# Kernel optimization log

Measured on AMD Instinct MI355X. Metric: run time of the kernel, lower is better.

## Reference

```python
import jax, jax.numpy as jnp
import numpy as np
import math

B, L, D, H = 4, 1024, 512, 8
TAU = 0.1
LN_EPS = 1e-5


def _attn(xq, xk, xv, wq, bq, wk, bk, wv, bv, wo, bo, energy=None, threshold=None):
    Bq, Lq, Dm = xq.shape
    Dh = Dm // H
    Q = (xq @ wq.T + bq).reshape(Bq, Lq, H, Dh)
    K = (xk @ wk.T + bk).reshape(Bq, -1, H, Dh)
    V = (xv @ wv.T + bv).reshape(Bq, -1, H, Dh)
    sc = jnp.einsum('bqhd,bkhd->bhqk', Q, K) / jnp.sqrt(jnp.float32(Dh))
    if energy is not None:
        # mask keys whose mean |energy| over channels is below threshold
        mask = jnp.abs(energy).mean(-1)[:, None, None, :] > threshold  # (B,1,1,Lk)
        sc = jnp.where(mask, sc, -jnp.inf)
    w = jnp.nan_to_num(jax.nn.softmax(sc, axis=-1))  # nan->0 for fully-masked rows
    o = jnp.einsum('bhqk,bkhd->bqhd', w, V).reshape(Bq, Lq, Dm)
    return o @ wo.T + bo


def _ln(x, w, b):
    m = x.mean(-1, keepdims=True)
    v = x.var(-1, keepdims=True)
    return (x - m) / jnp.sqrt(v + LN_EPS) * w + b


def _mlp(x, w1, b1, w2, b2):
    h = jax.nn.gelu(x @ w1.T + b1, approximate=False)  # torch nn.GELU default = exact
    return h @ w2.T + b2


def setup_inputs():
    key = jax.random.key(0)
    ks = list(jax.random.split(key, 64))

    def nxt():
        return ks.pop(0)

    def w(shape, scale=0.02):
        return jax.random.normal(nxt(), shape, dtype=jnp.float32) * scale

    inp = {
        'LL': jax.random.normal(nxt(), (B, D, L), dtype=jnp.float32),
        'LH': jax.random.normal(nxt(), (B, D, L), dtype=jnp.float32),
        'raw_tau': jnp.float32(math.log(TAU / (1.0 - TAU))),
    }
    for p in ('llA', 'lhA', 'crA'):
        for nm in ('q', 'k', 'v', 'o'):
            inp[f'{p}_w{nm}'] = w((D, D))
            inp[f'{p}_b{nm}'] = jnp.zeros((D,), jnp.float32)
    for p in ('mlp_ll', 'mlp_lh'):
        inp[f'{p}_w1'] = w((4 * D, D))
        inp[f'{p}_b1'] = jnp.zeros((4 * D,), jnp.float32)
        inp[f'{p}_w2'] = w((D, 4 * D))
        inp[f'{p}_b2'] = jnp.zeros((D,), jnp.float32)
    inp['n1_w'] = jnp.ones((D,), jnp.float32)
    inp['n1_b'] = jnp.zeros((D,), jnp.float32)
    inp['n2_w'] = jnp.ones((D,), jnp.float32)
    inp['n2_b'] = jnp.zeros((D,), jnp.float32)
    return inp


def reference(LL, LH, raw_tau,
              llA_wq, llA_bq, llA_wk, llA_bk, llA_wv, llA_bv, llA_wo, llA_bo,
              lhA_wq, lhA_bq, lhA_wk, lhA_bk, lhA_wv, lhA_bv, lhA_wo, lhA_bo,
              crA_wq, crA_bq, crA_wk, crA_bk, crA_wv, crA_bv, crA_wo, crA_bo,
              mlp_ll_w1, mlp_ll_b1, mlp_ll_w2, mlp_ll_b2,
              mlp_lh_w1, mlp_lh_b1, mlp_lh_w2, mlp_lh_b2,
              n1_w, n1_b, n2_w, n2_b):
    tau = jax.nn.sigmoid(raw_tau)
    ll_s = jnp.transpose(LL, (0, 2, 1))  # (B,L,D)
    lh_s = jnp.transpose(LH, (0, 2, 1))
    ll_o = _attn(ll_s, ll_s, ll_s, llA_wq, llA_bq, llA_wk, llA_bk, llA_wv, llA_bv, llA_wo, llA_bo)
    lh_o = _attn(lh_s, lh_s, lh_s, lhA_wq, lhA_bq, lhA_wk, lhA_bk, lhA_wv, lhA_bv, lhA_wo, lhA_bo,
                 energy=lh_s, threshold=tau)
    cr_o = _attn(ll_o, lh_o, lh_o, crA_wq, crA_bq, crA_wk, crA_bk, crA_wv, crA_bv, crA_wo, crA_bo)
    ll_f = _ln(ll_s + ll_o + cr_o, n1_w, n1_b)
    ll_f = _mlp(ll_f, mlp_ll_w1, mlp_ll_b1, mlp_ll_w2, mlp_ll_b2) + ll_f
    lh_f = _ln(lh_s + lh_o, n2_w, n2_b)
    lh_f = _mlp(lh_f, mlp_lh_w1, mlp_lh_b1, mlp_lh_w2, mlp_lh_b2) + lh_f
    return (jnp.transpose(ll_f, (0, 2, 1)), jnp.transpose(lh_f, (0, 2, 1)))
```

## Files before the change

### kernel.cpp

```cpp
#include <hip/hip_runtime.h>
#include <hip/hip_bf16.h>
#include <stdint.h>

typedef unsigned short u16;
typedef __bf16 bf16_t;
typedef bf16_t bf16x8 __attribute__((ext_vector_type(8)));
typedef float f32x4 __attribute__((ext_vector_type(4)));

#define DEV static __device__ __forceinline__

DEV u16 f2b(float f) {
    __hip_bfloat16 h = __float2bfloat16(f);
    return __builtin_bit_cast(u16, h);
}

DEV bf16x8 ld_frag(const u16* p) {
    uint4 u = *reinterpret_cast<const uint4*>(p);
    return __builtin_bit_cast(bf16x8, u);
}

DEV float gelu(float v) {
    float y = 0.79788456080286536f * (v + 0.044715f * v * v * v);
    float e = __expf(-2.f * fabsf(y));
    float th = (1.f - e) / (1.f + e);
    th = copysignf(th, y);
    return 0.5f * v * (1.f + th);
}

DEV void gl_lds16(const u16* g, u16* l) {
    __builtin_amdgcn_global_load_lds(
        (const __attribute__((address_space(1))) void*)(uintptr_t)g,
        (__attribute__((address_space(3))) void*)(unsigned int)(uintptr_t)l,
        16, 0, 0);
}

struct ConvEnt { const float* s; u16* d; int n; };
struct ConvArgs { ConvEnt e[16]; };

__global__ __launch_bounds__(256) void k_conv(ConvArgs a) {
    const ConvEnt en = a.e[blockIdx.y];
    for (int i = (blockIdx.x * 256 + threadIdx.x) * 4; i < en.n; i += 256 * 256 * 4) {
        const float4 f = *reinterpret_cast<const float4*>(en.s + i);
        unsigned r0 = (unsigned)f2b(f.x) | ((unsigned)f2b(f.y) << 16);
        unsigned r1 = (unsigned)f2b(f.z) | ((unsigned)f2b(f.w) << 16);
        uint2 rr; rr.x = r0; rr.y = r1;
        *reinterpret_cast<uint2*>(en.d + i) = rr;
    }
}

struct CpyEnt { const float* s; float* d; };
struct CpyArgs { CpyEnt e[8]; };

__global__ __launch_bounds__(256) void k_cpyf(CpyArgs a) {
    const CpyEnt en = a.e[blockIdx.y];
    int i = blockIdx.x * 256 + threadIdx.x;
    en.d[i] = en.s[i];
}

__global__ __launch_bounds__(256) void k_tin(const float* __restrict__ LL, const float* __restrict__ LH,
                                             float* __restrict__ llf, u16* __restrict__ llb,
                                             float* __restrict__ lhf, u16* __restrict__ lhb) {
    __shared__ float t[32][33];
    int z = blockIdx.z, b = z & 3;
    const float* in = (z < 4) ? LL : LH;
    float* of = (z < 4) ? llf : lhf;
    u16* ob = (z < 4) ? llb : lhb;
    int l0 = blockIdx.x * 32, d0 = blockIdx.y * 32;
    int tx = threadIdx.x, ty = threadIdx.y;
#pragma unroll
    for (int j = 0; j < 4; ++j) {
        int d = d0 + ty + j * 8;
        t[ty + j * 8][tx] = in[((size_t)b * 512 + d) * 1024 + l0 + tx];
    }
    __syncthreads();
#pragma unroll
    for (int j = 0; j < 4; ++j) {
        int l = l0 + ty + j * 8;
        float v = t[tx][ty + j * 8];
        size_t o = ((size_t)b * 1024 + l) * 512 + d0 + tx;
        of[o] = v;
        ob[o] = f2b(v);
    }
}

__global__ __launch_bounds__(256) void k_tout(const float* __restrict__ y0, const float* __restrict__ y1,
                                              float* __restrict__ out) {
    __shared__ float t[32][33];
    int z = blockIdx.z, b = z & 3;
    const float* in = (z < 4) ? y0 : y1;
    float* o = out + ((z < 4) ? 0 : (size_t)4096 * 512);
    int l0 = blockIdx.x * 32, d0 = blockIdx.y * 32;
    int tx = threadIdx.x, ty = threadIdx.y;
#pragma unroll
    for (int j = 0; j < 4; ++j) {
        int l = l0 + ty + j * 8;
        t[ty + j * 8][tx] = in[((size_t)b * 1024 + l) * 512 + d0 + tx];
    }
    __syncthreads();
#pragma unroll
    for (int j = 0; j < 4; ++j) {
        int d = d0 + ty + j * 8;
        o[((size_t)b * 512 + d) * 1024 + l0 + tx] = t[tx][ty + j * 8];
    }
}

__global__ __launch_bounds__(256) void k_mask(const float* __restrict__ lh_s,
                                              const float* __restrict__ raw_tau,
                                              float* __restrict__ kbias) {
    int row = blockIdx.x * 4 + (threadIdx.x >> 6);
    int lane = threadIdx.x & 63;
    const float* p = lh_s + (size_t)row * 512 + lane * 8;
    float s = 0.f;
#pragma unroll
    for (int j = 0; j < 8; ++j) s += fabsf(p[j]);
#pragma unroll
    for (int m = 32; m >= 1; m >>= 1) s += __shfl_xor(s, m, 64);
    float tau = 1.f / (1.f + expf(-raw_tau[0]));
    if (lane == 0) kbias[row] = (s * (1.f / 512.f) > tau) ? 0.f : -3.0e38f;
}

__global__ __launch_bounds__(256) void k_ln(const float* __restrict__ a, const float* __restrict__ b,
                                            const float* __restrict__ c, const float* __restrict__ w,
                                            const float* __restrict__ bi,
                                            float* __restrict__ of, u16* __restrict__ ob) {
    int row = blockIdx.x * 4 + (threadIdx.x >> 6);
    int lane = threadIdx.x & 63;
    size_t base = (size_t)row * 512 + lane * 8;
    float x[8];
#pragma unroll
    for (int j = 0; j < 8; ++j) {
        float v = a[base + j] + b[base + j];
        if (c) v += c[base + j];
        x[j] = v;
    }
    float s = 0.f, s2 = 0.f;
#pragma unroll
    for (int j = 0; j < 8; ++j) { s += x[j]; s2 += x[j] * x[j]; }
#pragma unroll
    for (int m = 32; m >= 1; m >>= 1) { s += __shfl_xor(s, m, 64); s2 += __shfl_xor(s2, m, 64); }
    float mean = s * (1.f / 512.f);
    float var = s2 * (1.f / 512.f) - mean * mean;
    float rs = rsqrtf(var + 1e-5f);
#pragma unroll
    for (int j = 0; j < 8; ++j) {
        float y = (x[j] - mean) * rs * w[lane * 8 + j] + bi[lane * 8 + j];
        of[base + j] = y;
        ob[base + j] = f2b(y);
    }
}

struct GP {
    const u16* A; const u16* W; const float* bias; const float* res;
    float* Cf; u16* Cb; u16* Qp; u16* Kp; u16* Vt;
    int N, K, kB, vB, nwg;
};

template <int BM, int BN, int GELU_ACT, int PACK>
__global__ __launch_bounds__(256) void k_gemm(GP p0, GP p1, int M) {
    constexpr int BK = 64;
    __shared__ alignas(16) u16 Al[2][BM * BK];
    __shared__ alignas(16) u16 Wl[2][BN * BK];
    GP g = (blockIdx.y == 0) ? p0 : p1;
    const int orig = blockIdx.x;
    if (orig >= g.nwg) return;
    int bid;
    {
        const int xcd = orig & 7, lin = orig >> 3;
        const int q = g.nwg >> 3, r = g.nwg & 7;
        bid = (xcd < r ? xcd * (q + 1) : r * (q + 1) + (xcd - r) * q) + lin;
    }
    const int K = g.K, N = g.N;
    const int nny = N / BN;
    const int m0 = (bid / nny) * BM, n0 = (bid % nny) * BN;

    const int t = threadIdx.x, w = t >> 6, l = t & 63;
    constexpr int FM = BM / 32, FN = BN / 32;
    const int wr = w >> 1, wc = w & 1;
    const int lq = l & 15, lg = l >> 4;
    f32x4 acc[FM][FN] = {};

    const int srow = l >> 3, schunk = l & 7;
    auto stage = [&](int kcol, int buf) {
#pragma unroll
        for (int i = 0; i < BM / 32; ++i) {
            const int row = i * 32 + w * 8 + srow;
            gl_lds16(g.A + (size_t)(m0 + row) * K + kcol + ((schunk ^ (row & 7)) * 8),
                     &Al[buf][(i * 32 + w * 8) * BK]);
        }
#pragma unroll
        for (int i = 0; i < BN / 32; ++i) {
            const int row = i * 32 + w * 8 + srow;
            gl_lds16(g.W + (size_t)(n0 + row) * K + kcol + ((schunk ^ (row & 7)) * 8),
                     &Wl[buf][(i * 32 + w * 8) * BK]);
        }
    };

    stage(0, 0);
    const int KT = K / BK;
    for (int kt = 0; kt < KT; ++kt) {
        const int cur = kt & 1;
        __syncthreads();
        if (kt + 1 < KT) stage((kt + 1) * BK, cur ^ 1);
#pragma unroll
        for (int s = 0; s < 2; ++s) {
            bf16x8 af[FM], bw[FN];
#pragma unroll
            for (int i = 0; i < FM; ++i) {
                const int row = wr * (BM / 2) + i * 16 + lq;
                af[i] = ld_frag(&Al[cur][row * BK + (((s * 4 + lg) ^ (row & 7)) * 8)]);
            }
#pragma unroll
            for (int j = 0; j < FN; ++j) {
                const int row = wc * (BN / 2) + j * 16 + lq;
                bw[j] = ld_frag(&Wl[cur][row * BK + (((s * 4 + lg) ^ (row & 7)) * 8)]);
            }
#pragma unroll
            for (int i = 0; i < FM; ++i)
#pragma unroll
                for (int j = 0; j < FN; ++j)
                    acc[i][j] = __builtin_amdgcn_mfma_f32_16x16x32_bf16(af[i], bw[j], acc[i][j], 0, 0, 0);
        }
    }

    if (PACK && n0 >= g.vB) {
        u16* T = (u16*)Al;
        constexpr int CH = BM / 8, CMASK = CH - 1, SH = (CH == 16) ? 4 : 3;
        __syncthreads();
#pragma unroll
        for (int i = 0; i < FM; ++i) {
#pragma unroll
            for (int j = 0; j < FN; ++j) {
                const int ni = wc * (BN / 2) + j * 16 + lq;
                const float bn = g.bias[n0 + ni];
#pragma unroll
                for (int r2 = 0; r2 < 4; ++r2) {
                    const int mi = wr * (BM / 2) + i * 16 + lg * 4 + r2;
                    T[ni * BM + (((mi >> 3) ^ (ni & CMASK)) * 8) + (mi & 7)] = f2b(acc[i][j][r2] + bn);
                }
            }
        }
        __syncthreads();
        const int bb = m0 >> 10, mloc = m0 & 1023;
        const int mc = t & CMASK, nib = t >> SH;
        constexpr int RPP = 256 / CH;
#pragma unroll
        for (int p2 = 0; p2 < BN / RPP; ++p2) {
            const int ni = nib + p2 * RPP;
            uint4 u = *reinterpret_cast<const uint4*>(&T[ni * BM + ((mc ^ (ni & CMASK)) * 8)]);
            const int d = n0 - g.vB + ni;
            *reinterpret_cast<uint4*>(
                &g.Vt[((size_t)(bb * 8 + (d >> 6)) * 64 + (d & 63)) * 1024 + mloc + mc * 8]) = u;
        }
        return;
    }

#pragma unroll
    for (int i = 0; i < FM; ++i) {
#pragma unroll
        for (int j = 0; j < FN; ++j) {
            const int n = n0 + wc * (BN / 2) + j * 16 + lq;
            const float bn = g.bias[n];
#pragma unroll
            for (int r2 = 0; r2 < 4; ++r2) {
                const int m = m0 + wr * (BM / 2) + i * 16 + lg * 4 + r2;
                float v = acc[i][j][r2] + bn;
                if (GELU_ACT) v = gelu(v);
                if (PACK) {
                    const int bb = m >> 10, ll_ = m & 1023;
                    if (n >= g.kB) {
                        const int d = n - g.kB;
                        g.Kp[((size_t)(bb * 8 + (d >> 6)) * 1024 + ll_) * 64 + (d & 63)] = f2b(v);
                    } else {
                        g.Qp[((size_t)(bb * 8 + (n >> 6)) * 1024 + ll_) * 64 + (n & 63)] = f2b(v * 0.125f);
                    }
                } else {
                    size_t o = (size_t)m * N + n;
                    if (g.res) v += g.res[o];
                    if (g.Cf) g.Cf[o] = v;
                    if (g.Cb) g.Cb[o] = f2b(v);
                }
            }
        }
    }
}

__global__ __launch_bounds__(256) void k_attn(const u16* __restrict__ Qp, const u16* __restrict__ Kp,
                                              const u16* __restrict__ Vtp, u16* __restrict__ O,
                                              const float* __restrict__ kbias, int nwg) {
    constexpr int L = 1024;
    __shared__ alignas(16) u16 Kl[2][64 * 64];
    __shared__ alignas(16) u16 Vl[2][64 * 64];
    __shared__ alignas(16) u16 Pl[128 * 64];
    const int t = threadIdx.x, w = t >> 6, l = t & 63;
    const int bid = ((int)blockIdx.x & 7) * (nwg >> 3) + ((int)blockIdx.x >> 3);
    const int bh = bid >> 3, q0 = (bid & 7) * 128;
    const int bz = bh >> 3, h = bh & 7;
    const int lq = l & 15, lg = l >> 4;
    const float* kb = (kbias != nullptr && bz >= 4) ? (kbias + (size_t)(bz - 4) * L) : nullptr;

    bf16x8 qa[2][2];
#pragma unroll
    for (int i = 0; i < 2; ++i) {
        const u16* qp = Qp + ((size_t)bh * L + q0 + w * 32 + i * 16 + lq) * 64 + lg * 8;
        qa[i][0] = ld_frag(qp);
        qa[i][1] = ld_frag(qp + 32);
    }

    const int r0 = w * 16 + (l >> 3), r1 = r0 + 8, c = l & 7;
    const u16* Ksrc0 = Kp + (size_t)bh * L * 64 + (size_t)r0 * 64 + ((c ^ (r0 & 7)) * 8);
    const u16* Ksrc1 = Kp + (size_t)bh * L * 64 + (size_t)r1 * 64 + ((c ^ (r1 & 7)) * 8);
    const u16* Vsrc0 = Vtp + (size_t)bh * 64 * L + (size_t)r0 * L + ((c ^ (r0 & 7)) * 8);
    const u16* Vsrc1 = Vtp + (size_t)bh * 64 * L + (size_t)r1 * L + ((c ^ (r1 & 7)) * 8);

    auto stage = [&](int k0, int buf) {
        gl_lds16(Ksrc0 + (size_t)k0 * 64, &Kl[buf][(w * 16) * 64]);
        gl_lds16(Ksrc1 + (size_t)k0 * 64, &Kl[buf][(w * 16 + 8) * 64]);
        gl_lds16(Vsrc0 + k0, &Vl[buf][(w * 16) * 64]);
        gl_lds16(Vsrc1 + k0, &Vl[buf][(w * 16 + 8) * 64]);
    };

    int addrA[4][2];
#pragma unroll
    for (int f = 0; f < 4; ++f) {
        int row = f * 16 + lq;
#pragma unroll
        for (int s = 0; s < 2; ++s) addrA[f][s] = row * 64 + (((s * 4 + lg) ^ (row & 7)) * 8);
    }
    int paddr[2][2], pwbase[2];
#pragma unroll
    for (int i = 0; i < 2; ++i) {
        const int prow = w * 32 + i * 16 + lq;
#pragma unroll
        for (int s = 0; s < 2; ++s) paddr[i][s] = prow * 64 + (((s * 4 + lg) ^ (prow & 7)) * 8);
        pwbase[i] = w * 32 + i * 16 + lg * 4;
    }

    f32x4 oacc[2][4] = {};
    float lrow[2][4] = {};

    stage(0, 0);
    for (int kt = 0; kt < 16; ++kt) {
        const int cur = kt & 1;
        __syncthreads();
        if (kt + 1 < 16) stage((kt + 1) * 64, cur ^ 1);

        f32x4 sc[2][4];
#pragma unroll
        for (int f = 0; f < 4; ++f) {
            bf16x8 k0 = ld_frag(&Kl[cur][addrA[f][0]]);
            bf16x8 k1 = ld_frag(&Kl[cur][addrA[f][1]]);
#pragma unroll
            for (int i = 0; i < 2; ++i) {
                f32x4 a = {};
                a = __builtin_amdgcn_mfma_f32_16x16x32_bf16(qa[i][0], k0, a, 0, 0, 0);
                a = __builtin_amdgcn_mfma_f32_16x16x32_bf16(qa[i][1], k1, a, 0, 0, 0);
                sc[i][f] = a;
            }
        }
#pragma unroll
        for (int f = 0; f < 4; ++f) {
            float bv = kb ? kb[kt * 64 + f * 16 + lq] : 0.f;
#pragma unroll
            for (int i = 0; i < 2; ++i) {
#pragma unroll
                for (int r = 0; r < 4; ++r) {
                    float pv = __expf(sc[i][f][r] + bv);
                    lrow[i][r] += pv;
                    const int prow = pwbase[i] + r;
                    Pl[prow * 64 + (((f * 2 + (lq >> 3)) ^ (prow & 7)) * 8) + (lq & 7)] = f2b(pv);
                }
            }
        }
        bf16x8 pa[2][2];
#pragma unroll
        for (int i = 0; i < 2; ++i) {
            pa[i][0] = ld_frag(&Pl[paddr[i][0]]);
            pa[i][1] = ld_frag(&Pl[paddr[i][1]]);
        }
#pragma unroll
        for (int db = 0; db < 4; ++db) {
            bf16x8 v0 = ld_frag(&Vl[cur][addrA[db][0]]);
            bf16x8 v1 = ld_frag(&Vl[cur][addrA[db][1]]);
#pragma unroll
            for (int i = 0; i < 2; ++i) {
                oacc[i][db] = __builtin_amdgcn_mfma_f32_16x16x32_bf16(pa[i][0], v0, oacc[i][db], 0, 0, 0);
                oacc[i][db] = __builtin_amdgcn_mfma_f32_16x16x32_bf16(pa[i][1], v1, oacc[i][db], 0, 0, 0);
            }
        }
    }
#pragma unroll
    for (int i = 0; i < 2; ++i)
#pragma unroll
        for (int r = 0; r < 4; ++r) {
            float v = lrow[i][r];
#pragma unroll
            for (int msk = 8; msk >= 1; msk >>= 1) v += __shfl_xor(v, msk, 16);
            lrow[i][r] = v;
        }
#pragma unroll
    for (int i = 0; i < 2; ++i) {
#pragma unroll
        for (int db = 0; db < 4; ++db) {
#pragma unroll
            for (int r = 0; r < 4; ++r) {
                float denom = lrow[i][r];
                float v = (denom > 0.f) ? oacc[i][db][r] / denom : 0.f;
                O[((size_t)bz * L + q0 + w * 32 + i * 16 + lg * 4 + r) * 512 + h * 64 + db * 16 + lq] = f2b(v);
            }
        }
    }
}

extern "C" void kernel_launch(void* const* d_in, const int* in_sizes, int n_in,
                              void* d_out, int out_size, void* d_ws, size_t ws_size,
                              hipStream_t stream) {
    const int M = 4096;
    const float* LL = (const float*)d_in[0];
    const float* LH = (const float*)d_in[1];
    const float* raw_tau = (const float*)d_in[2];
    auto F = [&](int i) { return (const float*)d_in[i]; };
    const int BIG = 1 << 28;

    char* p = (char*)d_ws;
    auto alloc = [&](size_t bytes) { void* r = (void*)p; p += (bytes + 255) & ~(size_t)255; return r; };
    const size_t MDf = (size_t)M * 512 * 4, MDb = (size_t)M * 512 * 2;
    float* ll_s_f = (float*)alloc(MDf);
    float* lh_s_f = (float*)alloc(MDf);
    u16* ll_s_b = (u16*)alloc(MDb);
    u16* lh_s_b = (u16*)alloc(MDb);
    u16* Qp = (u16*)alloc(2 * MDb);
    u16* Kp = (u16*)alloc(2 * MDb);
    u16* Vt = (u16*)alloc(2 * MDb);
    u16* Cxb = (u16*)alloc(2 * MDb);
    float* ll_o_f = (float*)alloc(MDf);
    u16* ll_o_b = (u16*)alloc(MDb);
    float* lh_o_f = (float*)alloc(MDf);
    u16* lh_o_b = (u16*)alloc(MDb);
    float* cr_o_f = (float*)alloc(MDf);
    float* ln_f_ll = (float*)alloc(MDf);
    float* ln_f_lh = (float*)alloc(MDf);
    u16* ln_b = (u16*)alloc(MDb);
    u16* hb = (u16*)alloc((size_t)M * 2048 * 2);
    float* yf_ll = (float*)alloc(MDf);
    float* yf_lh = (float*)alloc(MDf);
    float* kbias = (float*)alloc(4096 * 4);
    float* bqkv_ll = (float*)alloc(1536 * 4);
    float* bqkv_lh = (float*)alloc(1536 * 4);
    float* bkv_cr = (float*)alloc(1024 * 4);
    const size_t WDD = (size_t)262144;
    u16* wqkv_ll = (u16*)alloc(3 * WDD * 2);
    u16* wqkv_lh = (u16*)alloc(3 * WDD * 2);
    u16* wkv_cr = (u16*)alloc(2 * WDD * 2);
    u16* wq_cr = (u16*)alloc(WDD * 2);
    u16* wo_ll = (u16*)alloc(WDD * 2);
    u16* wo_lh = (u16*)alloc(WDD * 2);
    u16* wo_cr = (u16*)alloc(WDD * 2);
    u16* wm[4];
    for (int i = 0; i < 4; ++i) wm[i] = (u16*)alloc((size_t)1048576 * 2);

    const size_t SET = (size_t)4 * 8 * 1024 * 64;

    ConvArgs ca;
    ca.e[0] = {F(3), wqkv_ll, (int)WDD};
    ca.e[1] = {F(5), wqkv_ll + WDD, (int)WDD};
    ca.e[2] = {F(7), wqkv_ll + 2 * WDD, (int)WDD};
    ca.e[3] = {F(11), wqkv_lh, (int)WDD};
    ca.e[4] = {F(13), wqkv_lh + WDD, (int)WDD};
    ca.e[5] = {F(15), wqkv_lh + 2 * WDD, (int)WDD};
    ca.e[6] = {F(19), wq_cr, (int)WDD};
    ca.e[7] = {F(21), wkv_cr, (int)WDD};
    ca.e[8] = {F(23), wkv_cr + WDD, (int)WDD};
    ca.e[9] = {F(9), wo_ll, (int)WDD};
    ca.e[10] = {F(17), wo_lh, (int)WDD};
    ca.e[11] = {F(25), wo_cr, (int)WDD};
    ca.e[12] = {F(27), wm[0], 1048576};
    ca.e[13] = {F(29), wm[1], 1048576};
    ca.e[14] = {F(31), wm[2], 1048576};
    ca.e[15] = {F(33), wm[3], 1048576};
    k_conv<<<dim3(256, 16), 256, 0, stream>>>(ca);

    CpyArgs cp;
    cp.e[0] = {F(4), bqkv_ll};
    cp.e[1] = {F(6), bqkv_ll + 512};
    cp.e[2] = {F(8), bqkv_ll + 1024};
    cp.e[3] = {F(12), bqkv_lh};
    cp.e[4] = {F(14), bqkv_lh + 512};
    cp.e[5] = {F(16), bqkv_lh + 1024};
    cp.e[6] = {F(22), bkv_cr};
    cp.e[7] = {F(24), bkv_cr + 512};
    k_cpyf<<<dim3(2, 8), 256, 0, stream>>>(cp);

    k_tin<<<dim3(32, 16, 8), dim3(32, 8), 0, stream>>>(LL, LH, ll_s_f, ll_s_b, lh_s_f, lh_s_b);
    k_mask<<<dim3(1024), 256, 0, stream>>>(lh_s_f, raw_tau, kbias);

    auto gp = [&](const u16* A, const u16* W, const float* bias, int N, int K, int nwg) {
        GP g = {};
        g.A = A; g.W = W; g.bias = bias; g.N = N; g.K = K; g.nwg = nwg;
        g.kB = BIG; g.vB = BIG;
        return g;
    };

    {
        GP a = gp(ll_s_b, wqkv_ll, bqkv_ll, 1536, 512, 384);
        a.kB = 512; a.vB = 1024; a.Qp = Qp; a.Kp = Kp; a.Vt = Vt;
        GP b = gp(lh_s_b, wqkv_lh, bqkv_lh, 1536, 512, 384);
        b.kB = 512; b.vB = 1024; b.Qp = Qp + SET; b.Kp = Kp + SET; b.Vt = Vt + SET;
        k_gemm<128, 128, 0, 1><<<dim3(384, 2), 256, 0, stream>>>(a, b, M);
    }
    k_attn<<<dim3(512), 256, 0, stream>>>(Qp, Kp, Vt, Cxb, kbias, 512);
    {
        GP a = gp(Cxb, wo_ll, F(10), 512, 512, 512);
        a.Cf = ll_o_f; a.Cb = ll_o_b;
        GP b = gp(Cxb + SET, wo_lh, F(18), 512, 512, 512);
        b.Cf = lh_o_f; b.Cb = lh_o_b;
        k_gemm<64, 64, 0, 0><<<dim3(512, 2), 256, 0, stream>>>(a, b, M);
    }
    k_ln<<<dim3(1024), 256, 0, stream>>>(lh_s_f, lh_o_f, nullptr, F(37), F(38), ln_f_lh, ln_b);
    {
        GP a = gp(ln_b, wm[2], F(32), 2048, 512, 512);
        a.Cb = hb;
        k_gemm<128, 128, 1, 0><<<dim3(512, 1), 256, 0, stream>>>(a, a, M);
    }
    {
        GP a = gp(ll_o_b, wq_cr, F(20), 512, 512, 512);
        a.Qp = Qp;
        GP b = gp(lh_o_b, wkv_cr, bkv_cr, 1024, 512, 1024);
        b.kB = 0; b.vB = 512; b.Kp = Kp; b.Vt = Vt;
        k_gemm<64, 64, 0, 1><<<dim3(1024, 2), 256, 0, stream>>>(a, b, M);
    }
    k_attn<<<dim3(256), 256, 0, stream>>>(Qp, Kp, Vt, Cxb, nullptr, 256);
    {
        GP a = gp(Cxb, wo_cr, F(26), 512, 512, 512);
        a.Cf = cr_o_f;
        GP b = gp(hb, wm[3], F(34), 512, 2048, 512);
        b.Cf = yf_lh; b.res = ln_f_lh;
        k_gemm<64, 64, 0, 0><<<dim3(512, 2), 256, 0, stream>>>(a, b, M);
    }
    k_ln<<<dim3(1024), 256, 0, stream>>>(ll_s_f, ll_o_f, cr_o_f, F(35), F(36), ln_f_ll, ln_b);
    {
        GP a = gp(ln_b, wm[0], F(28), 2048, 512, 512);
        a.Cb = hb;
        k_gemm<128, 128, 1, 0><<<dim3(512, 1), 256, 0, stream>>>(a, a, M);
    }
    {
        GP a = gp(hb, wm[1], F(30), 512, 2048, 512);
        a.Cf = yf_ll; a.res = ln_f_ll;
        k_gemm<64, 64, 0, 0><<<dim3(512, 1), 256, 0, stream>>>(a, a, M);
    }
    k_tout<<<dim3(32, 16, 8), dim3(32, 8), 0, stream>>>(yf_ll, yf_lh, (float*)d_out);
}
```

Baseline: 268.7 us.

## Merge prep kernels, batch lh MLP up-proj with cross QKV, use exp2 softmax

```diff
diff --git a/kernel.cpp b/kernel.cpp
--- a/kernel.cpp
+++ b/kernel.cpp
@@ -8,6 +8,8 @@
 typedef float f32x4 __attribute__((ext_vector_type(4)));
 
 #define DEV static __device__ __forceinline__
+
+#define QSCALE 0.18033688011112042f
 
 DEV u16 f2b(float f) {
     __hip_bfloat16 h = __float2bfloat16(f);
@@ -35,57 +37,60 @@
 }
 
 struct ConvEnt { const float* s; u16* d; int n; };
-struct ConvArgs { ConvEnt e[16]; };
-
-__global__ __launch_bounds__(256) void k_conv(ConvArgs a) {
-    const ConvEnt en = a.e[blockIdx.y];
-    for (int i = (blockIdx.x * 256 + threadIdx.x) * 4; i < en.n; i += 256 * 256 * 4) {
-        const float4 f = *reinterpret_cast<const float4*>(en.s + i);
-        unsigned r0 = (unsigned)f2b(f.x) | ((unsigned)f2b(f.y) << 16);
-        unsigned r1 = (unsigned)f2b(f.z) | ((unsigned)f2b(f.w) << 16);
-        uint2 rr; rr.x = r0; rr.y = r1;
-        *reinterpret_cast<uint2*>(en.d + i) = rr;
-    }
-}
-
 struct CpyEnt { const float* s; float* d; };
-struct CpyArgs { CpyEnt e[8]; };
-
-__global__ __launch_bounds__(256) void k_cpyf(CpyArgs a) {
-    const CpyEnt en = a.e[blockIdx.y];
-    int i = blockIdx.x * 256 + threadIdx.x;
-    en.d[i] = en.s[i];
-}
-
-__global__ __launch_bounds__(256) void k_tin(const float* __restrict__ LL, const float* __restrict__ LH,
-                                             float* __restrict__ llf, u16* __restrict__ llb,
-                                             float* __restrict__ lhf, u16* __restrict__ lhb) {
-    __shared__ float t[32][33];
-    int z = blockIdx.z, b = z & 3;
-    const float* in = (z < 4) ? LL : LH;
-    float* of = (z < 4) ? llf : lhf;
-    u16* ob = (z < 4) ? llb : lhb;
-    int l0 = blockIdx.x * 32, d0 = blockIdx.y * 32;
-    int tx = threadIdx.x, ty = threadIdx.y;
-#pragma unroll
-    for (int j = 0; j < 4; ++j) {
-        int d = d0 + ty + j * 8;
-        t[ty + j * 8][tx] = in[((size_t)b * 512 + d) * 1024 + l0 + tx];
-    }
-    __syncthreads();
-#pragma unroll
-    for (int j = 0; j < 4; ++j) {
-        int l = l0 + ty + j * 8;
-        float v = t[tx][ty + j * 8];
-        size_t o = ((size_t)b * 1024 + l) * 512 + d0 + tx;
-        of[o] = v;
-        ob[o] = f2b(v);
+struct PreArgs {
+    const float* LL; const float* LH;
+    float* llf; u16* llb; float* lhf; u16* lhb;
+    ConvEnt ce[16];
+    CpyEnt pe[8];
+};
+
+__global__ __launch_bounds__(256) void k_pre(PreArgs a) {
+    __shared__ float tb[32][33];
+    const int bid = blockIdx.x, t = threadIdx.x;
+    if (bid < 4096) {
+        const int z = bid >> 9, gy = (bid >> 5) & 15, gx = bid & 31;
+        const int b = z & 3;
+        const float* in = (z < 4) ? a.LL : a.LH;
+        float* of = (z < 4) ? a.llf : a.lhf;
+        u16* ob = (z < 4) ? a.llb : a.lhb;
+        const int l0 = gx * 32, d0 = gy * 32;
+        const int tx = t & 31, ty = t >> 5;
+#pragma unroll
+        for (int j = 0; j < 4; ++j) {
+            int d = d0 + ty + j * 8;
+            tb[ty + j * 8][tx] = in[((size_t)b * 512 + d) * 1024 + l0 + tx];
+        }
+        __syncthreads();
+#pragma unroll
+        for (int j = 0; j < 4; ++j) {
+            int l = l0 + ty + j * 8;
+            float v = tb[tx][ty + j * 8];
+            size_t o = ((size_t)b * 1024 + l) * 512 + d0 + tx;
+            of[o] = v;
+            ob[o] = f2b(v);
+        }
+    } else if (bid < 8192) {
+        const int cb = bid - 4096;
+        const ConvEnt en = a.ce[cb >> 8];
+        for (int i = ((cb & 255) * 256 + t) * 4; i < en.n; i += 256 * 256 * 4) {
+            const float4 f = *reinterpret_cast<const float4*>(en.s + i);
+            unsigned r0 = (unsigned)f2b(f.x) | ((unsigned)f2b(f.y) << 16);
+            unsigned r1 = (unsigned)f2b(f.z) | ((unsigned)f2b(f.w) << 16);
+            uint2 rr; rr.x = r0; rr.y = r1;
+            *reinterpret_cast<uint2*>(en.d + i) = rr;
+        }
+    } else {
+        const int cb = bid - 8192;
+        const CpyEnt en = a.pe[cb >> 1];
+        const int i = (cb & 1) * 256 + t;
+        en.d[i] = en.s[i];
     }
 }
 
 __global__ __launch_bounds__(256) void k_tout(const float* __restrict__ y0, const float* __restrict__ y1,
                                               float* __restrict__ out) {
-    __shared__ float t[32][33];
+    __shared__ float tb[32][33];
     int z = blockIdx.z, b = z & 3;
     const float* in = (z < 4) ? y0 : y1;
     float* o = out + ((z < 4) ? 0 : (size_t)4096 * 512);
@@ -94,13 +99,13 @@
 #pragma unroll
     for (int j = 0; j < 4; ++j) {
         int l = l0 + ty + j * 8;
-        t[ty + j * 8][tx] = in[((size_t)b * 1024 + l) * 512 + d0 + tx];
+        tb[ty + j * 8][tx] = in[((size_t)b * 1024 + l) * 512 + d0 + tx];
     }
     __syncthreads();
 #pragma unroll
     for (int j = 0; j < 4; ++j) {
         int d = d0 + ty + j * 8;
-        o[((size_t)b * 512 + d) * 1024 + l0 + tx] = t[tx][ty + j * 8];
+        o[((size_t)b * 512 + d) * 1024 + l0 + tx] = tb[tx][ty + j * 8];
     }
 }
 
@@ -116,7 +121,7 @@
 #pragma unroll
     for (int m = 32; m >= 1; m >>= 1) s += __shfl_xor(s, m, 64);
     float tau = 1.f / (1.f + expf(-raw_tau[0]));
-    if (lane == 0) kbias[row] = (s * (1.f / 512.f) > tau) ? 0.f : -3.0e38f;
+    if (lane == 0) kbias[row] = (s * (1.f / 512.f) > tau) ? 0.f : -__builtin_inff();
 }
 
 __global__ __launch_bounds__(256) void k_ln(const float* __restrict__ a, const float* __restrict__ b,
@@ -152,15 +157,15 @@
 struct GP {
     const u16* A; const u16* W; const float* bias; const float* res;
     float* Cf; u16* Cb; u16* Qp; u16* Kp; u16* Vt;
-    int N, K, kB, vB, nwg;
+    int N, K, kB, vB, nwg, gelu, pack;
 };
 
-template <int BM, int BN, int GELU_ACT, int PACK>
-__global__ __launch_bounds__(256) void k_gemm(GP p0, GP p1, int M) {
+template <int BM, int BN>
+__global__ __launch_bounds__(256) void k_gemm(GP p0, GP p1, GP p2, int M) {
     constexpr int BK = 64;
     __shared__ alignas(16) u16 Al[2][BM * BK];
     __shared__ alignas(16) u16 Wl[2][BN * BK];
-    GP g = (blockIdx.y == 0) ? p0 : p1;
+    GP g = (blockIdx.y == 0) ? p0 : (blockIdx.y == 1) ? p1 : p2;
     const int orig = blockIdx.x;
     if (orig >= g.nwg) return;
     int bid;
@@ -222,7 +227,7 @@
         }
     }
 
-    if (PACK && n0 >= g.vB) {
+    if (g.pack && n0 >= g.vB) {
         u16* T = (u16*)Al;
         constexpr int CH = BM / 8, CMASK = CH - 1, SH = (CH == 16) ? 4 : 3;
         __syncthreads();
@@ -264,14 +269,14 @@
             for (int r2 = 0; r2 < 4; ++r2) {
                 const int m = m0 + wr * (BM / 2) + i * 16 + lg * 4 + r2;
                 float v = acc[i][j][r2] + bn;
-                if (GELU_ACT) v = gelu(v);
-                if (PACK) {
+                if (g.gelu) v = gelu(v);
+                if (g.pack) {
                     const int bb = m >> 10, ll_ = m & 1023;
                     if (n >= g.kB) {
                         const int d = n - g.kB;
                         g.Kp[((size_t)(bb * 8 + (d >> 6)) * 1024 + ll_) * 64 + (d & 63)] = f2b(v);
                     } else {
-                        g.Qp[((size_t)(bb * 8 + (n >> 6)) * 1024 + ll_) * 64 + (n & 63)] = f2b(v * 0.125f);
+                        g.Qp[((size_t)(bb * 8 + (n >> 6)) * 1024 + ll_) * 64 + (n & 63)] = f2b(v * QSCALE);
                     }
                 } else {
                     size_t o = (size_t)m * N + n;
@@ -345,6 +350,7 @@
         if (kt + 1 < 16) stage((kt + 1) * 64, cur ^ 1);
 
         f32x4 sc[2][4];
+        __builtin_amdgcn_s_setprio(1);
 #pragma unroll
         for (int f = 0; f < 4; ++f) {
             bf16x8 k0 = ld_frag(&Kl[cur][addrA[f][0]]);
@@ -357,6 +363,7 @@
                 sc[i][f] = a;
             }
         }
+        __builtin_amdgcn_s_setprio(0);
 #pragma unroll
         for (int f = 0; f < 4; ++f) {
             float bv = kb ? kb[kt * 64 + f * 16 + lq] : 0.f;
@@ -364,7 +371,7 @@
             for (int i = 0; i < 2; ++i) {
 #pragma unroll
                 for (int r = 0; r < 4; ++r) {
-                    float pv = __expf(sc[i][f][r] + bv);
+                    float pv = exp2f(sc[i][f][r] + bv);
                     lrow[i][r] += pv;
                     const int prow = pwbase[i] + r;
                     Pl[prow * 64 + (((f * 2 + (lq >> 3)) ^ (prow & 7)) * 8) + (lq & 7)] = f2b(pv);
@@ -377,6 +384,7 @@
             pa[i][0] = ld_frag(&Pl[paddr[i][0]]);
             pa[i][1] = ld_frag(&Pl[paddr[i][1]]);
         }
+        __builtin_amdgcn_s_setprio(1);
 #pragma unroll
         for (int db = 0; db < 4; ++db) {
             bf16x8 v0 = ld_frag(&Vl[cur][addrA[db][0]]);
@@ -387,6 +395,7 @@
                 oacc[i][db] = __builtin_amdgcn_mfma_f32_16x16x32_bf16(pa[i][1], v1, oacc[i][db], 0, 0, 0);
             }
         }
+        __builtin_amdgcn_s_setprio(0);
     }
 #pragma unroll
     for (int i = 0; i < 2; ++i)
@@ -460,52 +469,49 @@
 
     const size_t SET = (size_t)4 * 8 * 1024 * 64;
 
-    ConvArgs ca;
-    ca.e[0] = {F(3), wqkv_ll, (int)WDD};
-    ca.e[1] = {F(5), wqkv_ll + WDD, (int)WDD};
-    ca.e[2] = {F(7), wqkv_ll + 2 * WDD, (int)WDD};
-    ca.e[3] = {F(11), wqkv_lh, (int)WDD};
-    ca.e[4] = {F(13), wqkv_lh + WDD, (int)WDD};
-    ca.e[5] = {F(15), wqkv_lh + 2 * WDD, (int)WDD};
-    ca.e[6] = {F(19), wq_cr, (int)WDD};
-    ca.e[7] = {F(21), wkv_cr, (int)WDD};
-    ca.e[8] = {F(23), wkv_cr + WDD, (int)WDD};
-    ca.e[9] = {F(9), wo_ll, (int)WDD};
-    ca.e[10] = {F(17), wo_lh, (int)WDD};
-    ca.e[11] = {F(25), wo_cr, (int)WDD};
-    ca.e[12] = {F(27), wm[0], 1048576};
-    ca.e[13] = {F(29), wm[1], 1048576};
-    ca.e[14] = {F(31), wm[2], 1048576};
-    ca.e[15] = {F(33), wm[3], 1048576};
-    k_conv<<<dim3(256, 16), 256, 0, stream>>>(ca);
-
-    CpyArgs cp;
-    cp.e[0] = {F(4), bqkv_ll};
-    cp.e[1] = {F(6), bqkv_ll + 512};
-    cp.e[2] = {F(8), bqkv_ll + 1024};
-    cp.e[3] = {F(12), bqkv_lh};
-    cp.e[4] = {F(14), bqkv_lh + 512};
-    cp.e[5] = {F(16), bqkv_lh + 1024};
-    cp.e[6] = {F(22), bkv_cr};
-    cp.e[7] = {F(24), bkv_cr + 512};
-    k_cpyf<<<dim3(2, 8), 256, 0, stream>>>(cp);
-
-    k_tin<<<dim3(32, 16, 8), dim3(32, 8), 0, stream>>>(LL, LH, ll_s_f, ll_s_b, lh_s_f, lh_s_b);
+    PreArgs pa;
+    pa.LL = LL; pa.LH = LH;
+    pa.llf = ll_s_f; pa.llb = ll_s_b; pa.lhf = lh_s_f; pa.lhb = lh_s_b;
+    pa.ce[0] = {F(3), wqkv_ll, (int)WDD};
+    pa.ce[1] = {F(5), wqkv_ll + WDD, (int)WDD};
+    pa.ce[2] = {F(7), wqkv_ll + 2 * WDD, (int)WDD};
+    pa.ce[3] = {F(11), wqkv_lh, (int)WDD};
+    pa.ce[4] = {F(13), wqkv_lh + WDD, (int)WDD};
+    pa.ce[5] = {F(15), wqkv_lh + 2 * WDD, (int)WDD};
+    pa.ce[6] = {F(19), wq_cr, (int)WDD};
+    pa.ce[7] = {F(21), wkv_cr, (int)WDD};
+    pa.ce[8] = {F(23), wkv_cr + WDD, (int)WDD};
+    pa.ce[9] = {F(9), wo_ll, (int)WDD};
+    pa.ce[10] = {F(17), wo_lh, (int)WDD};
+    pa.ce[11] = {F(25), wo_cr, (int)WDD};
+    pa.ce[12] = {F(27), wm[0], 1048576};
+    pa.ce[13] = {F(29), wm[1], 1048576};
+    pa.ce[14] = {F(31), wm[2], 1048576};
+    pa.ce[15] = {F(33), wm[3], 1048576};
+    pa.pe[0] = {F(4), bqkv_ll};
+    pa.pe[1] = {F(6), bqkv_ll + 512};
+    pa.pe[2] = {F(8), bqkv_ll + 1024};
+    pa.pe[3] = {F(12), bqkv_lh};
+    pa.pe[4] = {F(14), bqkv_lh + 512};
+    pa.pe[5] = {F(16), bqkv_lh + 1024};
+    pa.pe[6] = {F(22), bkv_cr};
+    pa.pe[7] = {F(24), bkv_cr + 512};
+    k_pre<<<dim3(8208), 256, 0, stream>>>(pa);
     k_mask<<<dim3(1024), 256, 0, stream>>>(lh_s_f, raw_tau, kbias);
 
     auto gp = [&](const u16* A, const u16* W, const float* bias, int N, int K, int nwg) {
         GP g = {};
         g.A = A; g.W = W; g.bias = bias; g.N = N; g.K = K; g.nwg = nwg;
-        g.kB = BIG; g.vB = BIG;
+        g.kB = BIG; g.vB = BIG; g.gelu = 0; g.pack = 0;
         return g;
     };
 
     {
         GP a = gp(ll_s_b, wqkv_ll, bqkv_ll, 1536, 512, 384);
-        a.kB = 512; a.vB = 1024; a.Qp = Qp; a.Kp = Kp; a.Vt = Vt;
+        a.pack = 1; a.kB = 512; a.vB = 1024; a.Qp = Qp; a.Kp = Kp; a.Vt = Vt;
         GP b = gp(lh_s_b, wqkv_lh, bqkv_lh, 1536, 512, 384);
-        b.kB = 512; b.vB = 1024; b.Qp = Qp + SET; b.Kp = Kp + SET; b.Vt = Vt + SET;
-        k_gemm<128, 128, 0, 1><<<dim3(384, 2), 256, 0, stream>>>(a, b, M);
+        b.pack = 1; b.kB = 512; b.vB = 1024; b.Qp = Qp + SET; b.Kp = Kp + SET; b.Vt = Vt + SET;
+        k_gemm<128, 128><<<dim3(384, 2), 256, 0, stream>>>(a, b, b, M);
     }
     k_attn<<<dim3(512), 256, 0, stream>>>(Qp, Kp, Vt, Cxb, kbias, 512);
     {
@@ -513,20 +519,18 @@
         a.Cf = ll_o_f; a.Cb = ll_o_b;
         GP b = gp(Cxb + SET, wo_lh, F(18), 512, 512, 512);
         b.Cf = lh_o_f; b.Cb = lh_o_b;
-        k_gemm<64, 64, 0, 0><<<dim3(512, 2), 256, 0, stream>>>(a, b, M);
+        k_gemm<64, 64><<<dim3(512, 2), 256, 0, stream>>>(a, b, b, M);
     }
     k_ln<<<dim3(1024), 256, 0, stream>>>(lh_s_f, lh_o_f, nullptr, F(37), F(38), ln_f_lh, ln_b);
     {
-        GP a = gp(ln_b, wm[2], F(32), 2048, 512, 512);
-        a.Cb = hb;
-        k_gemm<128, 128, 1, 0><<<dim3(512, 1), 256, 0, stream>>>(a, a, M);
-    }
-    {
         GP a = gp(ll_o_b, wq_cr, F(20), 512, 512, 512);
+        a.pack = 1;
         a.Qp = Qp;
         GP b = gp(lh_o_b, wkv_cr, bkv_cr, 1024, 512, 1024);
-        b.kB = 0; b.vB = 512; b.Kp = Kp; b.Vt = Vt;
-        k_gemm<64, 64, 0, 1><<<dim3(1024, 2), 256, 0, stream>>>(a, b, M);
+        b.pack = 1; b.kB = 0; b.vB = 512; b.Kp = Kp; b.Vt = Vt;
+        GP cdsc = gp(ln_b, wm[2], F(32), 2048, 512, 2048);
+        cdsc.gelu = 1; cdsc.Cb = hb;
+        k_gemm<64, 64><<<dim3(2048, 3), 256, 0, stream>>>(a, b, cdsc, M);
     }
     k_attn<<<dim3(256), 256, 0, stream>>>(Qp, Kp, Vt, Cxb, nullptr, 256);
     {
@@ -534,18 +538,18 @@
         a.Cf = cr_o_f;
         GP b = gp(hb, wm[3], F(34), 512, 2048, 512);
         b.Cf = yf_lh; b.res = ln_f_lh;
-        k_gemm<64, 64, 0, 0><<<dim3(512, 2), 256, 0, stream>>>(a, b, M);
+        k_gemm<64, 64><<<dim3(512, 2), 256, 0, stream>>>(a, b, b, M);
     }
     k_ln<<<dim3(1024), 256, 0, stream>>>(ll_s_f, ll_o_f, cr_o_f, F(35), F(36), ln_f_ll, ln_b);
     {
         GP a = gp(ln_b, wm[0], F(28), 2048, 512, 512);
-        a.Cb = hb;
-        k_gemm<128, 128, 1, 0><<<dim3(512, 1), 256, 0, stream>>>(a, a, M);
+        a.gelu = 1; a.Cb = hb;
+        k_gemm<128, 128><<<dim3(512, 1), 256, 0, stream>>>(a, a, a, M);
     }
     {
         GP a = gp(hb, wm[1], F(30), 512, 2048, 512);
         a.Cf = yf_ll; a.res = ln_f_ll;
-        k_gemm<64, 64, 0, 0><<<dim3(512, 1), 256, 0, stream>>>(a, a, M);
+        k_gemm<64, 64><<<dim3(512, 1), 256, 0, stream>>>(a, a, a, M);
     }
     k_tout<<<dim3(32, 16, 8), dim3(32, 8), 0, stream>>>(yf_ll, yf_lh, (float*)d_out);
 }
```

Measured after the change: 284.1 us. +5.7%, slower.
